# Kernel optimization log

Hardware: AMD Instinct MI355X
Metric: run time of the kernel (lower is better)

## Reference

```python
import jax, jax.numpy as jnp
import numpy as np

CHANNELS = 10
LENGTH = 64
DEPTH = 4
BATCH = 2048


def setup_inputs() -> dict:
    key = jax.random.key(0)
    x = jax.random.normal(key, (BATCH, CHANNELS * LENGTH), dtype=jnp.float32)
    return {"x": x}


def _seg_exp(dx, depth):
    # Signature of a single linear segment with increment dx: (B, C).
    # Level k is dx^{(x)k} / k! (flattened to (B, C^k)).
    b = dx.shape[0]
    terms = [dx]
    for k in range(2, depth + 1):
        t = jnp.einsum('bi,bj->bij', terms[-1], dx).reshape(b, -1) / k
        terms.append(t)
    return tuple(terms)


def _chen(a, b, depth):
    # Truncated tensor-algebra product (Chen's identity), both with scalar part 1.
    # (A (x) B)_k = A_k + B_k + sum_{i=1}^{k-1} A_i (x) B_{k-i}
    bsz = a[0].shape[0]
    out = []
    for k in range(1, depth + 1):
        t = a[k - 1] + b[k - 1]
        for i in range(1, k):
            t = t + jnp.einsum('bi,bj->bij', a[i - 1], b[k - i - 1]).reshape(bsz, -1)
        out.append(t)
    return tuple(out)


def signature(path, depth):
    # path: (B, C, L). Increments along the path (last) dimension.
    dx = (path[:, :, 1:] - path[:, :, :-1]).transpose(0, 2, 1)  # (B, L-1, C)
    init = _seg_exp(dx[:, 0], depth)

    def step(carry, dxt):
        return _chen(carry, _seg_exp(dxt, depth), depth), None

    sig, _ = jax.lax.scan(step, init, dx[:, 1:].transpose(1, 0, 2))  # scan over L-2 steps
    return jnp.concatenate(sig, axis=-1)  # (B, sum_k C^k)


def reference(x):
    path = x.reshape(x.shape[0], CHANNELS, LENGTH)
    return signature(path, DEPTH)
```

## Files before the change

### kernel.cpp

```cpp
#include <hip/hip_runtime.h>
#include <hip/hip_bf16.h>


typedef short short8 __attribute__((ext_vector_type(8)));
typedef float f2 __attribute__((ext_vector_type(2)));
typedef float f4 __attribute__((ext_vector_type(4)));
typedef float f32x4 __attribute__((ext_vector_type(4)));
typedef unsigned int uint4v __attribute__((ext_vector_type(4)));

constexpr int C = 10, L = 64, T = 63;
constexpr int OUTSZ = 10 + 100 + 1000 + 10000;
constexpr int SP = 68;
constexpr int KS = 64;

__device__ __forceinline__ unsigned packbf(float lo, float hi) {
  union { __hip_bfloat162 h; unsigned u; } cv;
  cv.h = __float22bfloat162_rn(make_float2(lo, hi));
  return cv.u;
}
__device__ __forceinline__ int swz(int row, int k) {
  return row * KS + ((((k >> 3) ^ (row & 7)) << 3) | (k & 7));
}

__global__ __launch_bounds__(512, 6) void sig4_kernel(
    const float* __restrict__ x, float* __restrict__ out)
{
  __shared__ __align__(16) unsigned char smem_raw[52160];
  unsigned short* Ab  = (unsigned short*)smem_raw;
  unsigned short* Ub  = (unsigned short*)(smem_raw + 12800);
  unsigned short* B0b = (unsigned short*)(smem_raw + 25600);
  unsigned short* B1b = (unsigned short*)(smem_raw + 39680);
  float* dxT = (float*)(smem_raw + 46720);
  float* PsT = (float*)(smem_raw + 49440);

  const int t = threadIdx.x;
  const int w = t >> 6, lane = t & 63;
  const float* __restrict__ xb = x + (size_t)blockIdx.x * (C * L);
  float* __restrict__ ob = out + (size_t)blockIdx.x * OUTSZ;

  for (int i = t; i < C * SP; i += 512) {
    int c = i / SP, s = i - c * SP;
    float v = 0.f;
    if (s < T) v = xb[c * L + s + 1] - xb[c * L + s];
    dxT[i] = v;
  }
  __syncthreads();
  for (int c = w; c < C; c += 8) {
    float v = (lane > 0) ? dxT[c * SP + lane - 1] : 0.f;
    #pragma unroll
    for (int d = 1; d < 64; d <<= 1) {
      float y = __shfl_up(v, d);
      if (lane >= d) v += y;
    }
    PsT[c * SP + lane] = v;
  }
  if (t < 40) PsT[(t >> 2) * SP + 64 + (t & 3)] = 0.f;
  __syncthreads();

  if (t < 100) {
    const int i_ = t / 10, j_ = t - (t / 10) * 10;
    const float* dip = dxT + i_ * SP;
    const float* pp  = PsT + i_ * SP;
    const float* djp = dxT + j_ * SP;
    float s2 = 0.f;
    #pragma unroll
    for (int ch = 0; ch < 8; ++ch) {
      f4 d0 = *(const f4*)(dip + ch * 8), d1 = *(const f4*)(dip + ch * 8 + 4);
      f4 p0 = *(const f4*)(pp  + ch * 8), p1 = *(const f4*)(pp  + ch * 8 + 4);
      f4 e0 = *(const f4*)(djp + ch * 8), e1 = *(const f4*)(djp + ch * 8 + 4);
      float di[8] = {d0.x, d0.y, d0.z, d0.w, d1.x, d1.y, d1.z, d1.w};
      float pv[8] = {p0.x, p0.y, p0.z, p0.w, p1.x, p1.y, p1.z, p1.w};
      float dj[8] = {e0.x, e0.y, e0.z, e0.w, e1.x, e1.y, e1.z, e1.w};
      float bu[8], bv[8], zz[8];
      #pragma unroll
      for (int e = 0; e < 8; ++e) {
        bu[e] = fmaf(di[e], 0.25f, pv[e]) * (dj[e] * (1.f / 3.f));
        bv[e] = fmaf(di[e], (1.f / 3.f), pv[e]) * (dj[e] * 0.5f);
        zz[e] = fmaf(di[e], 0.5f, pv[e]) * dj[e];
      }
      float u2v[8], v2v[8];
      #pragma unroll
      for (int e = 0; e < 8; ++e) {
        u2v[e] = bu[e] + s2;
        v2v[e] = bv[e] + s2;
        s2 += zz[e];
      }
      uint4v vp, up;
      #pragma unroll
      for (int q = 0; q < 4; ++q) {
        vp[q] = packbf(v2v[2 * q], v2v[2 * q + 1]);
        up[q] = packbf(u2v[2 * q], u2v[2 * q + 1]);
      }
      *(uint4v*)&Ab[swz(t, ch * 8)] = vp;
      *(uint4v*)&Ub[swz(t, ch * 8)] = up;
    }
    ob[10 + t] = s2;
    if (j_ == 0) ob[i_] = PsT[i_ * SP + 63];
  } else if (t >= 128) {
    const int q = t - 128;
    for (int tt = q; tt < 1320; tt += 384) {
      if (tt < 880) {
        const int col = tt >> 3, ch = tt & 7, base = ch * 8;
        float bval[8];
        if (col < 100) {
          const int k2 = col / 10, l2 = col - (col / 10) * 10;
          const float* dk = dxT + k2 * SP;
          const float* pl = PsT + l2 * SP;
          const float S1l = pl[63];
          f4 d0 = *(const f4*)(dk + base), d1 = *(const f4*)(dk + base + 4);
          f4 pa = *(const f4*)(pl + base), pb = *(const f4*)(pl + base + 4);
          f4 pc = *(const f4*)(pl + base + 8);
          float dv[8] = {d0.x, d0.y, d0.z, d0.w, d1.x, d1.y, d1.z, d1.w};
          float Pn[8] = {pa.y, pa.z, pa.w, pb.x, pb.y, pb.z, pb.w, pc.x};
          #pragma unroll
          for (int e = 0; e < 8; ++e) bval[e] = dv[e] * (S1l - Pn[e]);
        } else {
          const float* dk = dxT + (col - 100) * SP;
          f4 d0 = *(const f4*)(dk + base), d1 = *(const f4*)(dk + base + 4);
          bval[0] = d0.x; bval[1] = d0.y; bval[2] = d0.z; bval[3] = d0.w;
          bval[4] = d1.x; bval[5] = d1.y; bval[6] = d1.z; bval[7] = d1.w;
        }
        uint4v pk;
        #pragma unroll
        for (int qq = 0; qq < 4; ++qq) pk[qq] = packbf(bval[2 * qq], bval[2 * qq + 1]);
        *(uint4v*)&B0b[swz(col, base)] = pk;
      } else {
        const int idx = tt - 880;
        const int col = idx >> 3, ch = idx & 7, base = ch * 8;
        float fs = sqrtf(8.f * (float)col + 1.f);
        int hi = (int)((fs - 1.f) * 0.5f);
        int tri = (hi * (hi + 1)) >> 1;
        if (col < tri) { --hi; tri = (hi * (hi + 1)) >> 1; }
        const int lo = col - tri;
        const float* dk = dxT + hi * SP;
        const float* dl = dxT + lo * SP;
        f4 a0 = *(const f4*)(dk + base), a1 = *(const f4*)(dk + base + 4);
        f4 c0 = *(const f4*)(dl + base), c1 = *(const f4*)(dl + base + 4);
        float bval[8] = {a0.x * c0.x * 0.5f, a0.y * c0.y * 0.5f,
                         a0.z * c0.z * 0.5f, a0.w * c0.w * 0.5f,
                         a1.x * c1.x * 0.5f, a1.y * c1.y * 0.5f,
                         a1.z * c1.z * 0.5f, a1.w * c1.w * 0.5f};
        uint4v pk;
        #pragma unroll
        for (int qq = 0; qq < 4; ++qq) pk[qq] = packbf(bval[2 * qq], bval[2 * qq + 1]);
        *(uint4v*)&B1b[swz(col, base)] = pk;
      }
    }
  }
  __syncthreads();

  if (w < 7) {
    const int lm = lane & 15, lg = lane >> 4;
    const int arow = w * 16 + lm;
    const short8 zf = {0, 0, 0, 0, 0, 0, 0, 0};
    short8 aV0 = (arow < 100) ? *(const short8*)&Ab[swz(arow, lg * 8)] : zf;
    short8 aV1 = (arow < 100) ? *(const short8*)&Ab[swz(arow, 32 + lg * 8)] : zf;
    short8 aU0 = (arow < 100) ? *(const short8*)&Ub[swz(arow, lg * 8)] : zf;
    short8 aU1 = (arow < 100) ? *(const short8*)&Ub[swz(arow, 32 + lg * 8)] : zf;
    f32x4 acc[7];
    #pragma unroll
    for (int ct = 0; ct < 7; ++ct) {
      const int bcol = ct * 16 + lm;
      short8 b00 = (bcol < 110) ? *(const short8*)&B0b[swz(bcol, lg * 8)] : zf;
      short8 b01 = (bcol < 110) ? *(const short8*)&B0b[swz(bcol, 32 + lg * 8)] : zf;
      short8 b10 = zf, b11 = zf;
      if (bcol < 100) {
        const int k2 = bcol / 10, l2 = bcol - k2 * 10;
        const int hi = (k2 > l2) ? k2 : l2;
        const int lo = (k2 > l2) ? l2 : k2;
        const int crow = ((hi * (hi + 1)) >> 1) + lo;
        b10 = *(const short8*)&B1b[swz(crow, lg * 8)];
        b11 = *(const short8*)&B1b[swz(crow, 32 + lg * 8)];
      }
      acc[ct] = f32x4{0.f, 0.f, 0.f, 0.f};
      acc[ct] = __builtin_amdgcn_mfma_f32_16x16x32_bf16(b00, aV0, acc[ct], 0, 0, 0);
      acc[ct] = __builtin_amdgcn_mfma_f32_16x16x32_bf16(b01, aV1, acc[ct], 0, 0, 0);
      acc[ct] = __builtin_amdgcn_mfma_f32_16x16x32_bf16(b10, aU0, acc[ct], 0, 0, 0);
      acc[ct] = __builtin_amdgcn_mfma_f32_16x16x32_bf16(b11, aU1, acc[ct], 0, 0, 0);
    }

    const int row = w * 16 + lm;
    if (row < 100) {
      float* rowp4 = ob + 1110 + row * 100;
      float* rowp3 = ob + 110 + row * 10;
      #pragma unroll
      for (int ct = 0; ct < 7; ++ct) {
        const int colbase = ct * 16 + lg * 4;
        f2 lo2 = {acc[ct][0], acc[ct][1]};
        f2 hi2 = {acc[ct][2], acc[ct][3]};
        if (colbase < 100) {
          *(f2*)(rowp4 + colbase) = lo2;
          *(f2*)(rowp4 + colbase + 2) = hi2;
        } else if (colbase < 110) {
          *(f2*)(rowp3 + (colbase - 100)) = lo2;
          if (colbase < 108) *(f2*)(rowp3 + (colbase - 98)) = hi2;
        }
      }
    }
  }
}

extern "C" void kernel_launch(void* const* d_in, const int* in_sizes, int n_in,
                              void* d_out, int out_size, void* d_ws, size_t ws_size,
                              hipStream_t stream) {
  const float* x = (const float*)d_in[0];
  float* out = (float*)d_out;
  const int batch = in_sizes[0] / (C * L);
  sig4_kernel<<<dim3(batch), dim3(512), 0, stream>>>(x, out);
}
```

Baseline: 32.97 us.

## Build B fragments in registers per wave and loop over row tiles

```diff
diff --git a/kernel.cpp b/kernel.cpp
--- a/kernel.cpp
+++ b/kernel.cpp
@@ -21,17 +21,17 @@
 __device__ __forceinline__ int swz(int row, int k) {
   return row * KS + ((((k >> 3) ^ (row & 7)) << 3) | (k & 7));
 }
+union frag_cast { uint4v u; short8 s; };
 
-__global__ __launch_bounds__(512, 6) void sig4_kernel(
+__global__ __launch_bounds__(512, 8) void sig4_kernel(
     const float* __restrict__ x, float* __restrict__ out)
 {
-  __shared__ __align__(16) unsigned char smem_raw[52160];
-  unsigned short* Ab  = (unsigned short*)smem_raw;
-  unsigned short* Ub  = (unsigned short*)(smem_raw + 12800);
-  unsigned short* B0b = (unsigned short*)(smem_raw + 25600);
-  unsigned short* B1b = (unsigned short*)(smem_raw + 39680);
-  float* dxT = (float*)(smem_raw + 46720);
-  float* PsT = (float*)(smem_raw + 49440);
+  __shared__ __align__(16) unsigned char smem_raw[33760];
+  unsigned short* Ab = (unsigned short*)smem_raw;
+  unsigned short* Ub = (unsigned short*)(smem_raw + 12800);
+  float* dxT = (float*)(smem_raw + 25600);
+  float* PsT = (float*)(smem_raw + 28320);
+  float* P1T = (float*)(smem_raw + 31040);
 
   const int t = threadIdx.x;
   const int w = t >> 6, lane = t & 63;
@@ -53,8 +53,9 @@
       if (lane >= d) v += y;
     }
     PsT[c * SP + lane] = v;
+    if (lane > 0) P1T[c * SP + lane - 1] = v;
+    if (lane == 63) P1T[c * SP + 63] = v;
   }
-  if (t < 40) PsT[(t >> 2) * SP + 64 + (t & 3)] = 0.f;
   __syncthreads();
 
   if (t < 100) {
@@ -96,102 +97,78 @@
     }
     ob[10 + t] = s2;
     if (j_ == 0) ob[i_] = PsT[i_ * SP + 63];
-  } else if (t >= 128) {
-    const int q = t - 128;
-    for (int tt = q; tt < 1320; tt += 384) {
-      if (tt < 880) {
-        const int col = tt >> 3, ch = tt & 7, base = ch * 8;
-        float bval[8];
-        if (col < 100) {
-          const int k2 = col / 10, l2 = col - (col / 10) * 10;
-          const float* dk = dxT + k2 * SP;
-          const float* pl = PsT + l2 * SP;
-          const float S1l = pl[63];
-          f4 d0 = *(const f4*)(dk + base), d1 = *(const f4*)(dk + base + 4);
-          f4 pa = *(const f4*)(pl + base), pb = *(const f4*)(pl + base + 4);
-          f4 pc = *(const f4*)(pl + base + 8);
-          float dv[8] = {d0.x, d0.y, d0.z, d0.w, d1.x, d1.y, d1.z, d1.w};
-          float Pn[8] = {pa.y, pa.z, pa.w, pb.x, pb.y, pb.z, pb.w, pc.x};
-          #pragma unroll
-          for (int e = 0; e < 8; ++e) bval[e] = dv[e] * (S1l - Pn[e]);
-        } else {
-          const float* dk = dxT + (col - 100) * SP;
-          f4 d0 = *(const f4*)(dk + base), d1 = *(const f4*)(dk + base + 4);
-          bval[0] = d0.x; bval[1] = d0.y; bval[2] = d0.z; bval[3] = d0.w;
-          bval[4] = d1.x; bval[5] = d1.y; bval[6] = d1.z; bval[7] = d1.w;
-        }
-        uint4v pk;
-        #pragma unroll
-        for (int qq = 0; qq < 4; ++qq) pk[qq] = packbf(bval[2 * qq], bval[2 * qq + 1]);
-        *(uint4v*)&B0b[swz(col, base)] = pk;
-      } else {
-        const int idx = tt - 880;
-        const int col = idx >> 3, ch = idx & 7, base = ch * 8;
-        float fs = sqrtf(8.f * (float)col + 1.f);
-        int hi = (int)((fs - 1.f) * 0.5f);
-        int tri = (hi * (hi + 1)) >> 1;
-        if (col < tri) { --hi; tri = (hi * (hi + 1)) >> 1; }
-        const int lo = col - tri;
-        const float* dk = dxT + hi * SP;
-        const float* dl = dxT + lo * SP;
-        f4 a0 = *(const f4*)(dk + base), a1 = *(const f4*)(dk + base + 4);
-        f4 c0 = *(const f4*)(dl + base), c1 = *(const f4*)(dl + base + 4);
-        float bval[8] = {a0.x * c0.x * 0.5f, a0.y * c0.y * 0.5f,
-                         a0.z * c0.z * 0.5f, a0.w * c0.w * 0.5f,
-                         a1.x * c1.x * 0.5f, a1.y * c1.y * 0.5f,
-                         a1.z * c1.z * 0.5f, a1.w * c1.w * 0.5f};
-        uint4v pk;
-        #pragma unroll
-        for (int qq = 0; qq < 4; ++qq) pk[qq] = packbf(bval[2 * qq], bval[2 * qq + 1]);
-        *(uint4v*)&B1b[swz(col, base)] = pk;
-      }
-    }
   }
   __syncthreads();
 
   if (w < 7) {
     const int lm = lane & 15, lg = lane >> 4;
-    const int arow = w * 16 + lm;
-    const short8 zf = {0, 0, 0, 0, 0, 0, 0, 0};
-    short8 aV0 = (arow < 100) ? *(const short8*)&Ab[swz(arow, lg * 8)] : zf;
-    short8 aV1 = (arow < 100) ? *(const short8*)&Ab[swz(arow, 32 + lg * 8)] : zf;
-    short8 aU0 = (arow < 100) ? *(const short8*)&Ub[swz(arow, lg * 8)] : zf;
-    short8 aU1 = (arow < 100) ? *(const short8*)&Ub[swz(arow, 32 + lg * 8)] : zf;
-    f32x4 acc[7];
-    #pragma unroll
-    for (int ct = 0; ct < 7; ++ct) {
-      const int bcol = ct * 16 + lm;
-      short8 b00 = (bcol < 110) ? *(const short8*)&B0b[swz(bcol, lg * 8)] : zf;
-      short8 b01 = (bcol < 110) ? *(const short8*)&B0b[swz(bcol, 32 + lg * 8)] : zf;
-      short8 b10 = zf, b11 = zf;
-      if (bcol < 100) {
-        const int k2 = bcol / 10, l2 = bcol - k2 * 10;
-        const int hi = (k2 > l2) ? k2 : l2;
-        const int lo = (k2 > l2) ? l2 : k2;
-        const int crow = ((hi * (hi + 1)) >> 1) + lo;
-        b10 = *(const short8*)&B1b[swz(crow, lg * 8)];
-        b11 = *(const short8*)&B1b[swz(crow, 32 + lg * 8)];
-      }
-      acc[ct] = f32x4{0.f, 0.f, 0.f, 0.f};
-      acc[ct] = __builtin_amdgcn_mfma_f32_16x16x32_bf16(b00, aV0, acc[ct], 0, 0, 0);
-      acc[ct] = __builtin_amdgcn_mfma_f32_16x16x32_bf16(b01, aV1, acc[ct], 0, 0, 0);
-      acc[ct] = __builtin_amdgcn_mfma_f32_16x16x32_bf16(b10, aU0, acc[ct], 0, 0, 0);
-      acc[ct] = __builtin_amdgcn_mfma_f32_16x16x32_bf16(b11, aU1, acc[ct], 0, 0, 0);
+    const int bcol = w * 16 + lm;
+    frag_cast B00, B01, B10, B11;
+    B00.u = uint4v{0, 0, 0, 0}; B01.u = uint4v{0, 0, 0, 0};
+    B10.u = uint4v{0, 0, 0, 0}; B11.u = uint4v{0, 0, 0, 0};
+    if (bcol < 100) {
+      const int k2 = bcol / 10, l2 = bcol - (bcol / 10) * 10;
+      const float* dk = dxT + k2 * SP;
+      const float* dl = dxT + l2 * SP;
+      const float* p1 = P1T + l2 * SP;
+      const float S1l = PsT[l2 * SP + 63];
+      f4 q0 = *(const f4*)(dk + lg * 8),      q1 = *(const f4*)(dk + lg * 8 + 4);
+      f4 q2 = *(const f4*)(dk + 32 + lg * 8), q3 = *(const f4*)(dk + 32 + lg * 8 + 4);
+      f4 r0 = *(const f4*)(p1 + lg * 8),      r1 = *(const f4*)(p1 + lg * 8 + 4);
+      f4 r2 = *(const f4*)(p1 + 32 + lg * 8), r3 = *(const f4*)(p1 + 32 + lg * 8 + 4);
+      f4 s0 = *(const f4*)(dl + lg * 8),      s1 = *(const f4*)(dl + lg * 8 + 4);
+      f4 s2v = *(const f4*)(dl + 32 + lg * 8), s3 = *(const f4*)(dl + 32 + lg * 8 + 4);
+      B00.u = uint4v{packbf(q0.x * (S1l - r0.x), q0.y * (S1l - r0.y)),
+                     packbf(q0.z * (S1l - r0.z), q0.w * (S1l - r0.w)),
+                     packbf(q1.x * (S1l - r1.x), q1.y * (S1l - r1.y)),
+                     packbf(q1.z * (S1l - r1.z), q1.w * (S1l - r1.w))};
+      B01.u = uint4v{packbf(q2.x * (S1l - r2.x), q2.y * (S1l - r2.y)),
+                     packbf(q2.z * (S1l - r2.z), q2.w * (S1l - r2.w)),
+                     packbf(q3.x * (S1l - r3.x), q3.y * (S1l - r3.y)),
+                     packbf(q3.z * (S1l - r3.z), q3.w * (S1l - r3.w))};
+      B10.u = uint4v{packbf(q0.x * s0.x * 0.5f, q0.y * s0.y * 0.5f),
+                     packbf(q0.z * s0.z * 0.5f, q0.w * s0.w * 0.5f),
+                     packbf(q1.x * s1.x * 0.5f, q1.y * s1.y * 0.5f),
+                     packbf(q1.z * s1.z * 0.5f, q1.w * s1.w * 0.5f)};
+      B11.u = uint4v{packbf(q2.x * s2v.x * 0.5f, q2.y * s2v.y * 0.5f),
+                     packbf(q2.z * s2v.z * 0.5f, q2.w * s2v.w * 0.5f),
+                     packbf(q3.x * s3.x * 0.5f, q3.y * s3.y * 0.5f),
+                     packbf(q3.z * s3.z * 0.5f, q3.w * s3.w * 0.5f)};
+    } else if (bcol < 110) {
+      const float* dk = dxT + (bcol - 100) * SP;
+      f4 q0 = *(const f4*)(dk + lg * 8),      q1 = *(const f4*)(dk + lg * 8 + 4);
+      f4 q2 = *(const f4*)(dk + 32 + lg * 8), q3 = *(const f4*)(dk + 32 + lg * 8 + 4);
+      B00.u = uint4v{packbf(q0.x, q0.y), packbf(q0.z, q0.w),
+                     packbf(q1.x, q1.y), packbf(q1.z, q1.w)};
+      B01.u = uint4v{packbf(q2.x, q2.y), packbf(q2.z, q2.w),
+                     packbf(q3.x, q3.y), packbf(q3.z, q3.w)};
     }
 
-    const int row = w * 16 + lm;
-    if (row < 100) {
-      float* rowp4 = ob + 1110 + row * 100;
-      float* rowp3 = ob + 110 + row * 10;
-      #pragma unroll
-      for (int ct = 0; ct < 7; ++ct) {
-        const int colbase = ct * 16 + lg * 4;
-        f2 lo2 = {acc[ct][0], acc[ct][1]};
-        f2 hi2 = {acc[ct][2], acc[ct][3]};
+    const int colbase = w * 16 + lg * 4;
+    const short8 zf = {0, 0, 0, 0, 0, 0, 0, 0};
+    #pragma unroll 1
+    for (int rt = 0; rt < 7; ++rt) {
+      const int arow = rt * 16 + lm;
+      short8 aV0 = (arow < 100) ? *(const short8*)&Ab[swz(arow, lg * 8)] : zf;
+      short8 aV1 = (arow < 100) ? *(const short8*)&Ab[swz(arow, 32 + lg * 8)] : zf;
+      short8 aU0 = (arow < 100) ? *(const short8*)&Ub[swz(arow, lg * 8)] : zf;
+      short8 aU1 = (arow < 100) ? *(const short8*)&Ub[swz(arow, 32 + lg * 8)] : zf;
+      f32x4 acc = {0.f, 0.f, 0.f, 0.f};
+      acc = __builtin_amdgcn_mfma_f32_16x16x32_bf16(B00.s, aV0, acc, 0, 0, 0);
+      acc = __builtin_amdgcn_mfma_f32_16x16x32_bf16(B01.s, aV1, acc, 0, 0, 0);
+      acc = __builtin_amdgcn_mfma_f32_16x16x32_bf16(B10.s, aU0, acc, 0, 0, 0);
+      acc = __builtin_amdgcn_mfma_f32_16x16x32_bf16(B11.s, aU1, acc, 0, 0, 0);
+
+      const int row = rt * 16 + lm;
+      if (row < 100) {
+        f2 lo2 = {acc[0], acc[1]};
+        f2 hi2 = {acc[2], acc[3]};
         if (colbase < 100) {
+          float* rowp4 = ob + 1110 + row * 100;
           *(f2*)(rowp4 + colbase) = lo2;
           *(f2*)(rowp4 + colbase + 2) = hi2;
         } else if (colbase < 110) {
+          float* rowp3 = ob + 110 + row * 10;
           *(f2*)(rowp3 + (colbase - 100)) = lo2;
           if (colbase < 108) *(f2*)(rowp3 + (colbase - 98)) = hi2;
         }
```

Result: faster. 30.68 us (-6.9%).
